# Kernel tuning notes

Measured on AMD Instinct MI355X. Metric: run time of the kernel, lower is better.

The kernel has to match this reference:

```python
import jax, jax.numpy as jnp
import numpy as np

N_EXPERTS = 64
TOP_K = 2
LOAD_BALANCE_COEF = 0.01
D_MODEL = 4096
N_TOKENS = 16384


def setup_inputs() -> dict:
    key = jax.random.key(0)
    kx, kw = jax.random.split(key)
    x = jax.random.normal(kx, (N_TOKENS, D_MODEL), dtype=jnp.float32)
    # nn.init.normal_(gate.weight, std=0.01); shape (n_experts, d_model)
    gate_w = 0.01 * jax.random.normal(kw, (N_EXPERTS, D_MODEL), dtype=jnp.float32)
    return {"x": x, "gate_w": gate_w}


def reference(x, gate_w):
    # logits: (N, n_experts)
    logits = jnp.einsum('nd,ed->ne', x, gate_w)
    router_probs = jax.nn.softmax(logits, axis=-1)
    top_k_weights, top_k_indices = jax.lax.top_k(router_probs, TOP_K)
    routing_weights = top_k_weights / jnp.sum(top_k_weights, axis=-1, keepdims=True)
    top1 = top_k_indices[:, 0]
    one_hot = jax.nn.one_hot(top1, N_EXPERTS, dtype=x.dtype)  # (N, n_experts)
    f_i = jnp.mean(one_hot, axis=0)          # fraction of tokens per expert (detached)
    p_i = jnp.mean(router_probs, axis=0)     # mean router prob per expert (diff.)
    load_balance_loss = LOAD_BALANCE_COEF * jnp.sum(jax.lax.stop_gradient(f_i) * p_i)
    return routing_weights, top_k_indices, load_balance_loss
```

## Files before the change

### kernel.cpp

```cpp
#include <hip/hip_runtime.h>
#include <hip/hip_bf16.h>
#include <math.h>

#define N_TOKENS 16384
#define D_MODEL  4096
#define N_EXP    64

#define BK     16
#define XS_LD  260
#define WS_LD  68
#define PB_BLOCKS 512

__global__ void __launch_bounds__(256)
router_gemm3(const float* __restrict__ x, const float* __restrict__ w,
             float* __restrict__ partial, int kslice) {
    __shared__ float xs[BK * XS_LD];
    __shared__ float ws[BK * WS_LD];

    int tid  = threadIdx.x;
    int tok0 = blockIdx.x * 256;
    int k0   = blockIdx.y * kslice;

    int wave = tid >> 6;
    int lane = tid & 63;
    int trow = wave * 64 + (lane & 7) * 8;
    int ecol = (lane >> 3) * 8;

    int s_sub = tid >> 2;
    int s_kc  = (tid & 3) * 4;

    float acc[8][8];
#pragma unroll
    for (int t = 0; t < 8; ++t)
#pragma unroll
        for (int e = 0; e < 8; ++e) acc[t][e] = 0.f;

    for (int kk = 0; kk < kslice; kk += BK) {
        const float* xsrc = x + (size_t)tok0 * D_MODEL + k0 + kk;
        const float* wsrc = w + k0 + kk;
        float4 xv0 = *(const float4*)(xsrc + (size_t)(s_sub +   0) * D_MODEL + s_kc);
        float4 xv1 = *(const float4*)(xsrc + (size_t)(s_sub +  64) * D_MODEL + s_kc);
        float4 xv2 = *(const float4*)(xsrc + (size_t)(s_sub + 128) * D_MODEL + s_kc);
        float4 xv3 = *(const float4*)(xsrc + (size_t)(s_sub + 192) * D_MODEL + s_kc);
        float4 wv  = *(const float4*)(wsrc + (size_t)s_sub * D_MODEL + s_kc);

        __syncthreads();

        xs[(s_kc + 0) * XS_LD + s_sub +   0] = xv0.x;
        xs[(s_kc + 1) * XS_LD + s_sub +   0] = xv0.y;
        xs[(s_kc + 2) * XS_LD + s_sub +   0] = xv0.z;
        xs[(s_kc + 3) * XS_LD + s_sub +   0] = xv0.w;
        xs[(s_kc + 0) * XS_LD + s_sub +  64] = xv1.x;
        xs[(s_kc + 1) * XS_LD + s_sub +  64] = xv1.y;
        xs[(s_kc + 2) * XS_LD + s_sub +  64] = xv1.z;
        xs[(s_kc + 3) * XS_LD + s_sub +  64] = xv1.w;
        xs[(s_kc + 0) * XS_LD + s_sub + 128] = xv2.x;
        xs[(s_kc + 1) * XS_LD + s_sub + 128] = xv2.y;
        xs[(s_kc + 2) * XS_LD + s_sub + 128] = xv2.z;
        xs[(s_kc + 3) * XS_LD + s_sub + 128] = xv2.w;
        xs[(s_kc + 0) * XS_LD + s_sub + 192] = xv3.x;
        xs[(s_kc + 1) * XS_LD + s_sub + 192] = xv3.y;
        xs[(s_kc + 2) * XS_LD + s_sub + 192] = xv3.z;
        xs[(s_kc + 3) * XS_LD + s_sub + 192] = xv3.w;
        ws[(s_kc + 0) * WS_LD + s_sub] = wv.x;
        ws[(s_kc + 1) * WS_LD + s_sub] = wv.y;
        ws[(s_kc + 2) * WS_LD + s_sub] = wv.z;
        ws[(s_kc + 3) * WS_LD + s_sub] = wv.w;

        __syncthreads();

#pragma unroll 4
        for (int k = 0; k < BK; ++k) {
            const float* xr = &xs[k * XS_LD + trow];
            const float* wr = &ws[k * WS_LD + ecol];
            float4 xa = *(const float4*)(xr);
            float4 xb = *(const float4*)(xr + 4);
            float4 wa = *(const float4*)(wr);
            float4 wb = *(const float4*)(wr + 4);
            float xf[8] = {xa.x, xa.y, xa.z, xa.w, xb.x, xb.y, xb.z, xb.w};
            float wf[8] = {wa.x, wa.y, wa.z, wa.w, wb.x, wb.y, wb.z, wb.w};
#pragma unroll
            for (int t = 0; t < 8; ++t)
#pragma unroll
                for (int e = 0; e < 8; ++e)
                    acc[t][e] = fmaf(xf[t], wf[e], acc[t][e]);
        }
    }

    float* po = partial + (size_t)blockIdx.y * (N_TOKENS * N_EXP)
                        + (size_t)(tok0 + trow) * N_EXP + ecol;
#pragma unroll
    for (int t = 0; t < 8; ++t) {
        *(float4*)(po + (size_t)t * N_EXP)     =
            make_float4(acc[t][0], acc[t][1], acc[t][2], acc[t][3]);
        *(float4*)(po + (size_t)t * N_EXP + 4) =
            make_float4(acc[t][4], acc[t][5], acc[t][6], acc[t][7]);
    }
}

__global__ void __launch_bounds__(256)
router_phaseB(const float* __restrict__ partial, int n_slices,
              float* __restrict__ out, float* __restrict__ block_sums) {
    __shared__ float p_acc[4][N_EXP];
    __shared__ float f_acc[4][N_EXP];

    int tid  = threadIdx.x;
    int wave = tid >> 6;
    int lane = tid & 63;

    p_acc[wave][lane] = 0.f;
    f_acc[wave][lane] = 0.f;

    for (int it = 0; it < 8; ++it) {
        int token = blockIdx.x * 32 + it * 4 + wave;

        float logit = 0.f;
        size_t base = (size_t)token * N_EXP + lane;
        for (int s = 0; s < n_slices; ++s)
            logit += partial[(size_t)s * (N_TOKENS * N_EXP) + base];

        float m = logit; int i1 = lane;
#pragma unroll
        for (int off = 1; off < 64; off <<= 1) {
            float ov = __shfl_xor(m, off, 64);
            int   oi = __shfl_xor(i1, off, 64);
            if (ov > m || (ov == m && oi < i1)) { m = ov; i1 = oi; }
        }

        float p = expf(logit - m);
        float denom = p;
#pragma unroll
        for (int off = 1; off < 64; off <<= 1)
            denom += __shfl_xor(denom, off, 64);

        p_acc[wave][lane] += p / denom;

        float l2 = (lane == i1) ? -__builtin_inff() : logit;
        int i2 = lane;
#pragma unroll
        for (int off = 1; off < 64; off <<= 1) {
            float ov = __shfl_xor(l2, off, 64);
            int   oi = __shfl_xor(i2, off, 64);
            if (ov > l2 || (ov == l2 && oi < i2)) { l2 = ov; i2 = oi; }
        }

        if (lane == i1) f_acc[wave][lane] += 1.f;

        if (lane == 0) {
            float p1 = 1.0f / denom;
            float p2 = expf(l2 - m) / denom;
            float s12 = p1 + p2;
            ((float2*)out)[token] = make_float2(p1 / s12, p2 / s12);
            ((float2*)(out + 2 * N_TOKENS))[token] =
                make_float2((float)i1, (float)i2);
        }
    }

    __syncthreads();
    if (tid < N_EXP) {
        float ps = p_acc[0][tid] + p_acc[1][tid] + p_acc[2][tid] + p_acc[3][tid];
        float fs = f_acc[0][tid] + f_acc[1][tid] + f_acc[2][tid] + f_acc[3][tid];
        block_sums[(size_t)blockIdx.x * 128 + tid]      = ps;
        block_sums[(size_t)blockIdx.x * 128 + 64 + tid] = fs;
    }
}

__global__ void __launch_bounds__(256)
router_final(const float* __restrict__ block_sums, float* __restrict__ out) {
    __shared__ float sp[4][N_EXP];
    __shared__ float sf[4][N_EXP];

    int tid  = threadIdx.x;
    int wave = tid >> 6;
    int lane = tid & 63;

    float ps = 0.f, fs = 0.f;
    for (int b = wave * (PB_BLOCKS / 4); b < (wave + 1) * (PB_BLOCKS / 4); ++b) {
        ps += block_sums[(size_t)b * 128 + lane];
        fs += block_sums[(size_t)b * 128 + 64 + lane];
    }
    sp[wave][lane] = ps;
    sf[wave][lane] = fs;
    __syncthreads();

    if (tid < N_EXP) {
        float pt = sp[0][tid] + sp[1][tid] + sp[2][tid] + sp[3][tid];
        float ft = sf[0][tid] + sf[1][tid] + sf[2][tid] + sf[3][tid];
        float v = pt * ft;
#pragma unroll
        for (int off = 1; off < 64; off <<= 1)
            v += __shfl_xor(v, off, 64);
        if (tid == 0)
            out[4 * N_TOKENS] = 0.01f * v / ((float)N_TOKENS * (float)N_TOKENS);
    }
}

extern "C" void kernel_launch(void* const* d_in, const int* in_sizes, int n_in,
                              void* d_out, int out_size, void* d_ws, size_t ws_size,
                              hipStream_t stream) {
    const float* x = (const float*)d_in[0];
    const float* w = (const float*)d_in[1];
    float* out = (float*)d_out;
    char* ws = (char*)d_ws;

    const size_t BS_BYTES = (size_t)PB_BLOCKS * 128 * sizeof(float);

    int ksplit = 1;
    for (int c = 16; c >= 1; c >>= 1) {
        size_t need = (size_t)c * N_TOKENS * N_EXP * sizeof(float) + BS_BYTES + 512;
        if (need <= ws_size) { ksplit = c; break; }
    }

    size_t partial_bytes = (size_t)ksplit * N_TOKENS * N_EXP * sizeof(float);
    float* partial = (float*)ws;
    float* block_sums = (float*)(ws + partial_bytes);

    dim3 gridA(N_TOKENS / 256, ksplit);
    router_gemm3<<<gridA, 256, 0, stream>>>(x, w, partial, D_MODEL / ksplit);

    router_phaseB<<<PB_BLOCKS, 256, 0, stream>>>(partial, ksplit, out, block_sums);

    router_final<<<1, 256, 0, stream>>>(block_sums, out);
}
```

Before: 448.7 us.

## Fuse router GEMM with softmax/top-k via in-block K-split across waves

Replaces the global split-K GEMM plus separate softmax/top-k kernel with one fused kernel. Each block handles 64 tokens, and each of its four waves covers a quarter of the K dimension with per-wave double-buffered shared tiles. Partial logits are reduced in shared memory and softmax/top-2 is computed in place, which removes the global partial-logit buffer round trip and one launch. Argmax now uses a fmax reduction plus ballot instead of paired value/index shuffles. The trade-off is smaller token tiles, so W is reloaded per 64 tokens, and the grid shrinks to 256 blocks.

```diff
diff --git a/kernel.cpp b/kernel.cpp
--- a/kernel.cpp
+++ b/kernel.cpp
@@ -1,165 +1,164 @@
 #include <hip/hip_runtime.h>
-#include <hip/hip_bf16.h>
 #include <math.h>
 
 #define N_TOKENS 16384
 #define D_MODEL  4096
 #define N_EXP    64
 
-#define BK     16
-#define XS_LD  260
-#define WS_LD  68
-#define PB_BLOCKS 512
+#define BK   16
+#define LD   68
+#define KW   (D_MODEL / 4)
+#define NT   (KW / BK)
+#define NBLK (N_TOKENS / 64)
 
 __global__ void __launch_bounds__(256)
-router_gemm3(const float* __restrict__ x, const float* __restrict__ w,
-             float* __restrict__ partial, int kslice) {
-    __shared__ float xs[BK * XS_LD];
-    __shared__ float ws[BK * WS_LD];
-
-    int tid  = threadIdx.x;
-    int tok0 = blockIdx.x * 256;
-    int k0   = blockIdx.y * kslice;
-
-    int wave = tid >> 6;
-    int lane = tid & 63;
-    int trow = wave * 64 + (lane & 7) * 8;
-    int ecol = (lane >> 3) * 8;
-
-    int s_sub = tid >> 2;
-    int s_kc  = (tid & 3) * 4;
-
-    float acc[8][8];
-#pragma unroll
-    for (int t = 0; t < 8; ++t)
-#pragma unroll
-        for (int e = 0; e < 8; ++e) acc[t][e] = 0.f;
-
-    for (int kk = 0; kk < kslice; kk += BK) {
-        const float* xsrc = x + (size_t)tok0 * D_MODEL + k0 + kk;
-        const float* wsrc = w + k0 + kk;
-        float4 xv0 = *(const float4*)(xsrc + (size_t)(s_sub +   0) * D_MODEL + s_kc);
-        float4 xv1 = *(const float4*)(xsrc + (size_t)(s_sub +  64) * D_MODEL + s_kc);
-        float4 xv2 = *(const float4*)(xsrc + (size_t)(s_sub + 128) * D_MODEL + s_kc);
-        float4 xv3 = *(const float4*)(xsrc + (size_t)(s_sub + 192) * D_MODEL + s_kc);
-        float4 wv  = *(const float4*)(wsrc + (size_t)s_sub * D_MODEL + s_kc);
-
-        __syncthreads();
-
-        xs[(s_kc + 0) * XS_LD + s_sub +   0] = xv0.x;
-        xs[(s_kc + 1) * XS_LD + s_sub +   0] = xv0.y;
-        xs[(s_kc + 2) * XS_LD + s_sub +   0] = xv0.z;
-        xs[(s_kc + 3) * XS_LD + s_sub +   0] = xv0.w;
-        xs[(s_kc + 0) * XS_LD + s_sub +  64] = xv1.x;
-        xs[(s_kc + 1) * XS_LD + s_sub +  64] = xv1.y;
-        xs[(s_kc + 2) * XS_LD + s_sub +  64] = xv1.z;
-        xs[(s_kc + 3) * XS_LD + s_sub +  64] = xv1.w;
-        xs[(s_kc + 0) * XS_LD + s_sub + 128] = xv2.x;
-        xs[(s_kc + 1) * XS_LD + s_sub + 128] = xv2.y;
-        xs[(s_kc + 2) * XS_LD + s_sub + 128] = xv2.z;
-        xs[(s_kc + 3) * XS_LD + s_sub + 128] = xv2.w;
-        xs[(s_kc + 0) * XS_LD + s_sub + 192] = xv3.x;
-        xs[(s_kc + 1) * XS_LD + s_sub + 192] = xv3.y;
-        xs[(s_kc + 2) * XS_LD + s_sub + 192] = xv3.z;
-        xs[(s_kc + 3) * XS_LD + s_sub + 192] = xv3.w;
-        ws[(s_kc + 0) * WS_LD + s_sub] = wv.x;
-        ws[(s_kc + 1) * WS_LD + s_sub] = wv.y;
-        ws[(s_kc + 2) * WS_LD + s_sub] = wv.z;
-        ws[(s_kc + 3) * WS_LD + s_sub] = wv.w;
-
-        __syncthreads();
-
-#pragma unroll 4
+router_fused(const float* __restrict__ x, const float* __restrict__ w,
+             float* __restrict__ out, float* __restrict__ block_sums) {
+    __shared__ float smem[4 * 4 * BK * LD + 2 * 4 * N_EXP];
+
+    const int tid  = threadIdx.x;
+    const int wv   = tid >> 6;
+    const int lane = tid & 63;
+    const int tok0 = blockIdx.x * 64;
+
+    float* xs  = smem + wv * (4 * BK * LD);
+    float* wsb = xs + 2 * BK * LD;
+
+    const int srow = lane >> 2;
+    const int skc  = (lane & 3) * 4;
+
+    const int tg   = lane & 7;
+    const int eg   = lane >> 3;
+    const int trow = tg * 8;
+    const int ecol = eg * 8;
+
+    const float* xp = x + (size_t)(tok0 + srow) * D_MODEL + (size_t)wv * KW + skc;
+    const float* wp = w + (size_t)srow * D_MODEL + (size_t)wv * KW + skc;
+
+    float acc[8][8] = {};
+
+#define LOADR(q, roff) (*(const float4*)((q) + (size_t)(roff) * D_MODEL))
+#define STORE_TILE(buf, v, roff) do {                      \
+        (buf)[(skc + 0) * LD + srow + (roff)] = (v).x;     \
+        (buf)[(skc + 1) * LD + srow + (roff)] = (v).y;     \
+        (buf)[(skc + 2) * LD + srow + (roff)] = (v).z;     \
+        (buf)[(skc + 3) * LD + srow + (roff)] = (v).w;     \
+    } while (0)
+
+    {
+        float4 a0 = LOADR(xp, 0),  a1 = LOADR(xp, 16);
+        float4 a2 = LOADR(xp, 32), a3 = LOADR(xp, 48);
+        float4 b0 = LOADR(wp, 0),  b1 = LOADR(wp, 16);
+        float4 b2 = LOADR(wp, 32), b3 = LOADR(wp, 48);
+        STORE_TILE(xs, a0, 0);  STORE_TILE(xs, a1, 16);
+        STORE_TILE(xs, a2, 32); STORE_TILE(xs, a3, 48);
+        STORE_TILE(wsb, b0, 0);  STORE_TILE(wsb, b1, 16);
+        STORE_TILE(wsb, b2, 32); STORE_TILE(wsb, b3, 48);
+    }
+
+    auto compute_tile = [&](const float* xb, const float* wb) {
+#pragma unroll
         for (int k = 0; k < BK; ++k) {
-            const float* xr = &xs[k * XS_LD + trow];
-            const float* wr = &ws[k * WS_LD + ecol];
-            float4 xa = *(const float4*)(xr);
-            float4 xb = *(const float4*)(xr + 4);
-            float4 wa = *(const float4*)(wr);
-            float4 wb = *(const float4*)(wr + 4);
-            float xf[8] = {xa.x, xa.y, xa.z, xa.w, xb.x, xb.y, xb.z, xb.w};
-            float wf[8] = {wa.x, wa.y, wa.z, wa.w, wb.x, wb.y, wb.z, wb.w};
-#pragma unroll
-            for (int t = 0; t < 8; ++t)
-#pragma unroll
-                for (int e = 0; e < 8; ++e)
-                    acc[t][e] = fmaf(xf[t], wf[e], acc[t][e]);
+            const float* xr = xb + k * LD + trow;
+            const float* wr = wb + k * LD + ecol;
+            float4 xa = *(const float4*)xr;
+            float4 xc = *(const float4*)(xr + 4);
+            float4 wa = *(const float4*)wr;
+            float4 wc = *(const float4*)(wr + 4);
+            float xf[8] = {xa.x, xa.y, xa.z, xa.w, xc.x, xc.y, xc.z, xc.w};
+            float wf[8] = {wa.x, wa.y, wa.z, wa.w, wc.x, wc.y, wc.z, wc.w};
+#pragma unroll
+            for (int i = 0; i < 8; ++i)
+#pragma unroll
+                for (int j = 0; j < 8; ++j)
+                    acc[i][j] = fmaf(xf[i], wf[j], acc[i][j]);
         }
-    }
-
-    float* po = partial + (size_t)blockIdx.y * (N_TOKENS * N_EXP)
-                        + (size_t)(tok0 + trow) * N_EXP + ecol;
-#pragma unroll
-    for (int t = 0; t < 8; ++t) {
-        *(float4*)(po + (size_t)t * N_EXP)     =
-            make_float4(acc[t][0], acc[t][1], acc[t][2], acc[t][3]);
-        *(float4*)(po + (size_t)t * N_EXP + 4) =
-            make_float4(acc[t][4], acc[t][5], acc[t][6], acc[t][7]);
-    }
-}
-
-__global__ void __launch_bounds__(256)
-router_phaseB(const float* __restrict__ partial, int n_slices,
-              float* __restrict__ out, float* __restrict__ block_sums) {
-    __shared__ float p_acc[4][N_EXP];
-    __shared__ float f_acc[4][N_EXP];
-
-    int tid  = threadIdx.x;
-    int wave = tid >> 6;
-    int lane = tid & 63;
-
-    p_acc[wave][lane] = 0.f;
-    f_acc[wave][lane] = 0.f;
-
-    for (int it = 0; it < 8; ++it) {
-        int token = blockIdx.x * 32 + it * 4 + wave;
-
-        float logit = 0.f;
-        size_t base = (size_t)token * N_EXP + lane;
-        for (int s = 0; s < n_slices; ++s)
-            logit += partial[(size_t)s * (N_TOKENS * N_EXP) + base];
-
-        float m = logit; int i1 = lane;
-#pragma unroll
-        for (int off = 1; off < 64; off <<= 1) {
-            float ov = __shfl_xor(m, off, 64);
-            int   oi = __shfl_xor(i1, off, 64);
-            if (ov > m || (ov == m && oi < i1)) { m = ov; i1 = oi; }
-        }
+    };
+
+#pragma unroll 2
+    for (int t = 0; t < NT - 1; ++t) {
+        float* xb = xs  + (t & 1) * (BK * LD);
+        float* wb = wsb + (t & 1) * (BK * LD);
+        float* xn = xs  + ((t + 1) & 1) * (BK * LD);
+        float* wn = wsb + ((t + 1) & 1) * (BK * LD);
+
+        const float* xq = xp + (t + 1) * BK;
+        const float* wq = wp + (t + 1) * BK;
+        float4 a0 = LOADR(xq, 0),  a1 = LOADR(xq, 16);
+        float4 a2 = LOADR(xq, 32), a3 = LOADR(xq, 48);
+        float4 b0 = LOADR(wq, 0),  b1 = LOADR(wq, 16);
+        float4 b2 = LOADR(wq, 32), b3 = LOADR(wq, 48);
+
+        compute_tile(xb, wb);
+
+        STORE_TILE(xn, a0, 0);  STORE_TILE(xn, a1, 16);
+        STORE_TILE(xn, a2, 32); STORE_TILE(xn, a3, 48);
+        STORE_TILE(wn, b0, 0);  STORE_TILE(wn, b1, 16);
+        STORE_TILE(wn, b2, 32); STORE_TILE(wn, b3, 48);
+    }
+    compute_tile(xs + ((NT - 1) & 1) * (BK * LD), wsb + ((NT - 1) & 1) * (BK * LD));
+
+    __syncthreads();
+
+    float* tile = smem + wv * 4096;
+#pragma unroll
+    for (int i = 0; i < 8; ++i) {
+        *(float4*)&tile[(trow + i) * 64 + ecol] =
+            make_float4(acc[i][0], acc[i][1], acc[i][2], acc[i][3]);
+        *(float4*)&tile[(trow + i) * 64 + ecol + 4] =
+            make_float4(acc[i][4], acc[i][5], acc[i][6], acc[i][7]);
+    }
+    __syncthreads();
+
+    float p_acc = 0.f, f_acc = 0.f;
+#pragma unroll 1
+    for (int it = 0; it < 16; ++it) {
+        const int tl = wv * 16 + it;
+        const int o  = tl * 64 + lane;
+        float logit = smem[o] + smem[4096 + o] + smem[8192 + o] + smem[12288 + o];
+
+        float m = logit;
+#pragma unroll
+        for (int off = 32; off; off >>= 1)
+            m = fmaxf(m, __shfl_xor(m, off, 64));
+        unsigned long long b1 = __ballot(logit == m);
+        int i1 = __ffsll(b1) - 1;
 
         float p = expf(logit - m);
         float denom = p;
 #pragma unroll
-        for (int off = 1; off < 64; off <<= 1)
+        for (int off = 32; off; off >>= 1)
             denom += __shfl_xor(denom, off, 64);
 
-        p_acc[wave][lane] += p / denom;
-
-        float l2 = (lane == i1) ? -__builtin_inff() : logit;
-        int i2 = lane;
-#pragma unroll
-        for (int off = 1; off < 64; off <<= 1) {
-            float ov = __shfl_xor(l2, off, 64);
-            int   oi = __shfl_xor(i2, off, 64);
-            if (ov > l2 || (ov == l2 && oi < i2)) { l2 = ov; i2 = oi; }
-        }
-
-        if (lane == i1) f_acc[wave][lane] += 1.f;
+        p_acc += p / denom;
+        if (lane == i1) f_acc += 1.f;
+
+        float lx = (lane == i1) ? -__builtin_inff() : logit;
+        float m2 = lx;
+#pragma unroll
+        for (int off = 32; off; off >>= 1)
+            m2 = fmaxf(m2, __shfl_xor(m2, off, 64));
+        unsigned long long b2 = __ballot(lx == m2);
+        int i2 = __ffsll(b2) - 1;
 
         if (lane == 0) {
             float p1 = 1.0f / denom;
-            float p2 = expf(l2 - m) / denom;
+            float p2 = expf(m2 - m) / denom;
             float s12 = p1 + p2;
+            int token = tok0 + tl;
             ((float2*)out)[token] = make_float2(p1 / s12, p2 / s12);
             ((float2*)(out + 2 * N_TOKENS))[token] =
                 make_float2((float)i1, (float)i2);
         }
     }
 
+    float* pf = smem + 4 * 4 * BK * LD;
+    pf[wv * 64 + lane]       = p_acc;
+    pf[256 + wv * 64 + lane] = f_acc;
     __syncthreads();
     if (tid < N_EXP) {
-        float ps = p_acc[0][tid] + p_acc[1][tid] + p_acc[2][tid] + p_acc[3][tid];
-        float fs = f_acc[0][tid] + f_acc[1][tid] + f_acc[2][tid] + f_acc[3][tid];
+        float ps = pf[tid] + pf[64 + tid] + pf[128 + tid] + pf[192 + tid];
+        float fs = pf[256 + tid] + pf[320 + tid] + pf[384 + tid] + pf[448 + tid];
         block_sums[(size_t)blockIdx.x * 128 + tid]      = ps;
         block_sums[(size_t)blockIdx.x * 128 + 64 + tid] = fs;
     }
@@ -171,16 +170,17 @@
     __shared__ float sf[4][N_EXP];
 
     int tid  = threadIdx.x;
-    int wave = tid >> 6;
+    int wv   = tid >> 6;
     int lane = tid & 63;
 
     float ps = 0.f, fs = 0.f;
-    for (int b = wave * (PB_BLOCKS / 4); b < (wave + 1) * (PB_BLOCKS / 4); ++b) {
+#pragma unroll 8
+    for (int b = wv * (NBLK / 4); b < (wv + 1) * (NBLK / 4); ++b) {
         ps += block_sums[(size_t)b * 128 + lane];
         fs += block_sums[(size_t)b * 128 + 64 + lane];
     }
-    sp[wave][lane] = ps;
-    sf[wave][lane] = fs;
+    sp[wv][lane] = ps;
+    sf[wv][lane] = fs;
     __syncthreads();
 
     if (tid < N_EXP) {
@@ -198,27 +198,12 @@
 extern "C" void kernel_launch(void* const* d_in, const int* in_sizes, int n_in,
                               void* d_out, int out_size, void* d_ws, size_t ws_size,
                               hipStream_t stream) {
+    (void)in_sizes; (void)n_in; (void)out_size; (void)ws_size;
     const float* x = (const float*)d_in[0];
     const float* w = (const float*)d_in[1];
     float* out = (float*)d_out;
-    char* ws = (char*)d_ws;
-
-    const size_t BS_BYTES = (size_t)PB_BLOCKS * 128 * sizeof(float);
-
-    int ksplit = 1;
-    for (int c = 16; c >= 1; c >>= 1) {
-        size_t need = (size_t)c * N_TOKENS * N_EXP * sizeof(float) + BS_BYTES + 512;
-        if (need <= ws_size) { ksplit = c; break; }
-    }
-
-    size_t partial_bytes = (size_t)ksplit * N_TOKENS * N_EXP * sizeof(float);
-    float* partial = (float*)ws;
-    float* block_sums = (float*)(ws + partial_bytes);
-
-    dim3 gridA(N_TOKENS / 256, ksplit);
-    router_gemm3<<<gridA, 256, 0, stream>>>(x, w, partial, D_MODEL / ksplit);
-
-    router_phaseB<<<PB_BLOCKS, 256, 0, stream>>>(partial, ksplit, out, block_sums);
-
+    float* block_sums = (float*)d_ws;
+
+    router_fused<<<NBLK, 256, 0, stream>>>(x, w, out, block_sums);
     router_final<<<1, 256, 0, stream>>>(block_sums, out);
 }
```

Result: faster. 420.1 us (-6.4%).
